# Performance work log

Hardware: AMD Instinct MI355X
Metric: run time of the kernel (lower is better)

## Reference

```python
import jax, jax.numpy as jnp
import numpy as np


def conv3x3(y, w, b):
    # y: [1, Cin, H, W], w: [Cout, Cin, 3, 3] -> [1, Cout, H, W], stride 1, pad 1
    out = jax.lax.conv_general_dilated(
        y, w, window_strides=(1, 1), padding='SAME',
        dimension_numbers=('NCHW', 'OIHW', 'NCHW'))
    return out + b[None, :, None, None]


def setup_inputs() -> dict:
    key = jax.random.key(0)
    ks = jax.random.split(key, 8)
    N, Cin, Cy, H, W, inter = 1024, 1024, 256, 128, 128, 256
    x = jax.random.normal(ks[0], (N, Cin), dtype=jnp.float32)
    y = jax.random.normal(ks[1], (1, Cy, H, W), dtype=jnp.float32)
    # weights initialized ~N(0, 0.01) as in the torch module; biases zero
    g_w = jax.random.normal(ks[2], (inter, Cy, 3, 3), dtype=jnp.float32) * 0.01
    g_b = jnp.zeros((inter,), dtype=jnp.float32)
    phi_w = jax.random.normal(ks[3], (inter, Cy, 3, 3), dtype=jnp.float32) * 0.01
    phi_b = jnp.zeros((inter,), dtype=jnp.float32)
    theta_w = jax.random.normal(ks[4], (inter, Cin), dtype=jnp.float32) * 0.01
    theta_b = jnp.zeros((inter,), dtype=jnp.float32)
    concat_w = jax.random.normal(ks[5], (1, 2 * inter, 1, 1), dtype=jnp.float32) * 0.01
    gamma = jnp.ones((1,), dtype=jnp.float32)  # torch inits 0; use 1 for nontrivial output
    return {"x": x, "y": y, "g_w": g_w, "g_b": g_b, "phi_w": phi_w,
            "phi_b": phi_b, "theta_w": theta_w, "theta_b": theta_b,
            "concat_w": concat_w, "gamma": gamma}


def reference(x, y, g_w, g_b, phi_w, phi_b, theta_w, theta_b, concat_w, gamma):
    inter = g_w.shape[0]
    H, W = y.shape[2], y.shape[3]
    g_y = conv3x3(y, g_w, g_b)          # [1, inter, H, W]
    phi_y = conv3x3(y, phi_w, phi_b)    # [1, inter, H, W]
    theta_x = x @ theta_w.T + theta_b   # [N, inter]
    # 1x1 conv over cat([theta repeated, phi repeated], dim=1) decomposes exactly
    # (linearity of the 1x1 conv, no bias) into two dot products + broadcast add,
    # avoiding the [N, 2*inter, H, W] materialization.
    w = concat_w[0, :, 0, 0]            # [2*inter]
    w_t, w_p = w[:inter], w[inter:]
    s_theta = theta_x @ w_t             # [N]
    s_phi = jnp.einsum('chw,c->hw', phi_y[0], w_p).reshape(-1)  # [H*W]
    f = jax.nn.softmax(s_theta[:, None] + s_phi[None, :], axis=1)  # [N, H*W]
    # g_y.squeeze() -> [inter,H,W]; permute(1,2,0).view(H*W, inter)
    g_flat = jnp.transpose(g_y[0], (1, 2, 0)).reshape(H * W, inter)
    z = gamma * (f @ g_flat)            # [N, inter]
    return z
```

## Files before the change

### kernel.cpp

```cpp
#include <hip/hip_runtime.h>

#define HWDIM 128
#define NPIX  (HWDIM * HWDIM)
#define CY    256
#define INTER 256
#define KTAPS 9
#define WEN   (CY * KTAPS)
#define NPART 64
#define NW1   8
#define NRG   4


__device__ __forceinline__ float wave_red_sum(float v) {
    #pragma unroll
    for (int s = 32; s > 0; s >>= 1) v += __shfl_down(v, s, 64);
    return v;
}
__device__ __forceinline__ float wave_red_max(float v) {
    #pragma unroll
    for (int s = 32; s > 0; s >>= 1) v = fmaxf(v, __shfl_down(v, s, 64));
    return v;
}

__global__ void k1_wepart(const float* __restrict__ phi_w,
                          const float* __restrict__ concat_w,
                          float* __restrict__ we_part) {
    int b = blockIdx.x, t = threadIdx.x;
    int og = b >> 3, cg = b & 7;
    int o = og * 256 + t;
    const float* pw = phi_w + o;
    float acc = 0.f;
    #pragma unroll 8
    for (int c = cg * 32; c < cg * 32 + 32; ++c)
        acc = fmaf(concat_w[INTER + c], pw[c * WEN], acc);
    we_part[cg * WEN + o] = acc;
}

template <int CPG>
__global__ void k2a_taps(const float* __restrict__ y,
                         const float* __restrict__ we_part,
                         float* __restrict__ A_part) {
    __shared__ float swe[CPG * KTAPS];
    int t = threadIdx.x;
    int pg = blockIdx.x & 63;
    int cg = blockIdx.x >> 6;

    for (int i = t; i < CPG * KTAPS; i += 256) {
        float s = 0.f;
        #pragma unroll
        for (int p = 0; p < NW1; ++p)
            s += we_part[p * WEN + cg * CPG * KTAPS + i];
        swe[i] = s;
    }
    __syncthreads();

    int pix = pg * 256 + t;
    float acc[KTAPS];
    #pragma unroll
    for (int k = 0; k < KTAPS; ++k) acc[k] = 0.f;

    const float* yp = y + (size_t)cg * CPG * NPIX + pix;
    #pragma unroll 4
    for (int ch = 0; ch < CPG; ++ch) {
        float yv = yp[ch * NPIX];
        const float* wk = swe + ch * KTAPS;
        #pragma unroll
        for (int k = 0; k < KTAPS; ++k)
            acc[k] = fmaf(wk[k], yv, acc[k]);
    }
    #pragma unroll
    for (int k = 0; k < KTAPS; ++k)
        A_part[(size_t)(cg * KTAPS + k) * NPIX + pix] = acc[k];
}

template <int NCS>
__global__ void k2b_sphi(const float* __restrict__ A_part,
                         float* __restrict__ sphi,
                         float* __restrict__ partials) {
    __shared__ float s4[4];
    __shared__ float sM;
    int t = threadIdx.x, wid = t >> 6, lane = t & 63;
    int pix = blockIdx.x * 256 + t;
    int h = pix >> 7, w = pix & 127;

    float acc = 0.f;
    #pragma unroll
    for (int kh = 0; kh < 3; ++kh) {
        int hh = h + kh - 1;
        if ((unsigned)hh >= (unsigned)HWDIM) continue;
        #pragma unroll
        for (int kw = 0; kw < 3; ++kw) {
            int ww = w + kw - 1;
            if ((unsigned)ww >= (unsigned)HWDIM) continue;
            int idx = hh * HWDIM + ww;
            int k = kh * 3 + kw;
            #pragma unroll
            for (int cg = 0; cg < NCS; ++cg)
                acc += A_part[(size_t)(cg * KTAPS + k) * NPIX + idx];
        }
    }
    sphi[pix] = acc;

    float m = wave_red_max(acc);
    if (lane == 0) s4[wid] = m;
    __syncthreads();
    if (t == 0) sM = fmaxf(fmaxf(s4[0], s4[1]), fmaxf(s4[2], s4[3]));
    __syncthreads();
    float M = sM;
    float e = expf(acc - M);
    float s = wave_red_sum(e);
    if (lane == 0) s4[wid] = s;
    __syncthreads();
    if (t == 0) {
        partials[2 * blockIdx.x]     = M;
        partials[2 * blockIdx.x + 1] = s4[0] + s4[1] + s4[2] + s4[3];
    }
}

__global__ void k3b_merge(const float* __restrict__ partials,
                          float* __restrict__ MS) {
    int t = threadIdx.x;
    float m = partials[2 * t], s = partials[2 * t + 1];
    float mr = wave_red_max(m);
    float M = __shfl(mr, 0, 64);
    float sv = s * expf(m - M);
    float S = wave_red_sum(sv);
    if (t == 0) { MS[0] = M; MS[1] = 1.f / S; }
}

__global__ void k4_q(const float* __restrict__ y,
                     const float* __restrict__ sphi,
                     const float* __restrict__ MS,
                     float* __restrict__ q_part) {
    __shared__ float sp[34 * 130];
    __shared__ float sq4[4][KTAPS];
    int cy = blockIdx.x & 255;
    int rg = blockIdx.x >> 8;
    int t = threadIdx.x;

    float M = MS[0], invS = MS[1];

    for (int i = t; i < 34 * 130; i += 256) {
        int r = i / 130, col = i - r * 130;
        int gr = rg * 32 + r - 1, gc = col - 1;
        float v = 0.f;
        if ((unsigned)gr < HWDIM && (unsigned)gc < HWDIM)
            v = expf(sphi[gr * HWDIM + gc] - M) * invS;
        sp[i] = v;
    }
    __syncthreads();

    const float* yc = y + (size_t)cy * NPIX;
    float acc[KTAPS];
    #pragma unroll
    for (int k = 0; k < KTAPS; ++k) acc[k] = 0.f;
    int c = t & 127, vg = t >> 7;

    for (int j = 0; j < 4; ++j) {
        int lr0 = vg * 4 + j * 8;
        float pv[6][3];
        #pragma unroll
        for (int u = 0; u < 6; ++u)
            #pragma unroll
            for (int v = 0; v < 3; ++v)
                pv[u][v] = sp[(lr0 + u) * 130 + c + v];
        #pragma unroll
        for (int dr = 0; dr < 4; ++dr) {
            float yv = yc[(rg * 32 + lr0 + dr) * HWDIM + c];
            #pragma unroll
            for (int kh = 0; kh < 3; ++kh)
                #pragma unroll
                for (int kw = 0; kw < 3; ++kw)
                    acc[kh * 3 + kw] = fmaf(pv[dr + 2 - kh][2 - kw], yv,
                                            acc[kh * 3 + kw]);
        }
    }

    int wid = t >> 6, lane = t & 63;
    #pragma unroll
    for (int k = 0; k < KTAPS; ++k) {
        float v = wave_red_sum(acc[k]);
        if (lane == 0) sq4[wid][k] = v;
    }
    __syncthreads();
    if (t < KTAPS)
        q_part[rg * WEN + cy * KTAPS + t] =
            sq4[0][t] + sq4[1][t] + sq4[2][t] + sq4[3][t];
}

__global__ void k5_row(const float* __restrict__ g_w,
                       const float* __restrict__ g_b,
                       const float* __restrict__ gamma,
                       const float* __restrict__ q_part,
                       float* __restrict__ row) {
    __shared__ float sq[WEN];
    __shared__ float s4[4];
    int t = threadIdx.x, c = blockIdx.x;
    for (int i = t; i < WEN; i += 256) {
        float s = 0.f;
        #pragma unroll
        for (int rg = 0; rg < NRG; ++rg) s += q_part[rg * WEN + i];
        sq[i] = s;
    }
    __syncthreads();

    const float* gw = g_w + (size_t)c * WEN;
    float acc = 0.f;
    for (int o = t; o < WEN; o += 256) acc = fmaf(gw[o], sq[o], acc);
    float v = wave_red_sum(acc);
    int wid = t >> 6, lane = t & 63;
    if (lane == 0) s4[wid] = v;
    __syncthreads();
    if (t == 0) row[c] = gamma[0] * (g_b[c] + s4[0] + s4[1] + s4[2] + s4[3]);
}

__global__ void k6_bcast(const float* __restrict__ row, float* __restrict__ out,
                         int out_size) {
    __shared__ float sr[256];
    sr[threadIdx.x] = row[threadIdx.x];
    __syncthreads();
    int gid = blockIdx.x * 256 + threadIdx.x;
    if (gid < out_size) out[gid] = sr[threadIdx.x];
}

extern "C" void kernel_launch(void* const* d_in, const int* in_sizes, int n_in,
                              void* d_out, int out_size, void* d_ws, size_t ws_size,
                              hipStream_t stream) {
    const float* y        = (const float*)d_in[1];
    const float* g_w      = (const float*)d_in[2];
    const float* g_b      = (const float*)d_in[3];
    const float* phi_w    = (const float*)d_in[4];
    const float* concat_w = (const float*)d_in[8];
    const float* gamma    = (const float*)d_in[9];
    float* out = (float*)d_out;

    const bool big = ws_size >= (size_t)(6u << 20);
    const int  ncs = big ? 8 : 2;

    float* ws       = (float*)d_ws;
    float* we_part  = ws;
    float* A_part   = we_part + NW1 * WEN;
    float* sphi     = A_part + (size_t)ncs * KTAPS * NPIX;
    float* partials = sphi + NPIX;
    float* MS       = partials + 2 * NPART;
    float* q_part   = MS + 16;
    float* row      = q_part + NRG * WEN;
    (void)in_sizes; (void)n_in;

    hipLaunchKernelGGL(k1_wepart, dim3(72), dim3(256), 0, stream,
                       phi_w, concat_w, we_part);
    if (big)
        hipLaunchKernelGGL(k2a_taps<32>,  dim3(64 * 8), dim3(256), 0, stream,
                           y, we_part, A_part);
    else
        hipLaunchKernelGGL(k2a_taps<128>, dim3(64 * 2), dim3(256), 0, stream,
                           y, we_part, A_part);
    if (big)
        hipLaunchKernelGGL(k2b_sphi<8>, dim3(NPART), dim3(256), 0, stream,
                           A_part, sphi, partials);
    else
        hipLaunchKernelGGL(k2b_sphi<2>, dim3(NPART), dim3(256), 0, stream,
                           A_part, sphi, partials);
    hipLaunchKernelGGL(k3b_merge, dim3(1), dim3(64), 0, stream, partials, MS);
    hipLaunchKernelGGL(k4_q, dim3(NRG * CY), dim3(256), 0, stream,
                       y, sphi, MS, q_part);
    hipLaunchKernelGGL(k5_row, dim3(CY), dim3(256), 0, stream,
                       g_w, g_b, gamma, q_part, row);
    hipLaunchKernelGGL(k6_bcast, dim3((out_size + 255) / 256), dim3(256), 0,
                       stream, row, out, out_size);
}
```

Baseline: 121.1 us.

## Widen grids, fold softmax merge into q kernel, split row reduction

Raises parallelism across the small kernels. The phi-weight partial sums now use 288 blocks instead of 72, the s_phi stage uses 256 blocks with four waves splitting the channel groups, and the row reduction uses 512 blocks with two halves that the broadcast kernel combines. The separate single-block softmax-merge kernel is removed; each k4 block now redoes the merge of the 256 (max, sum) partials itself, which removes one launch but repeats that small reduction in every block. The small-workspace fallback path is dropped, so the code now always assumes the large workspace.

```diff
diff --git a/kernel.cpp b/kernel.cpp
--- a/kernel.cpp
+++ b/kernel.cpp
@@ -6,8 +6,10 @@
 #define INTER 256
 #define KTAPS 9
 #define WEN   (CY * KTAPS)
-#define NPART 64
-#define NW1   8
+#define NW1   32
+#define NCS   8
+#define CPG   32
+#define NPART2 256
 #define NRG   4
 
 
@@ -26,20 +28,21 @@
                           const float* __restrict__ concat_w,
                           float* __restrict__ we_part) {
     int b = blockIdx.x, t = threadIdx.x;
-    int og = b >> 3, cg = b & 7;
+    int cg = b / 9, og = b - cg * 9;
     int o = og * 256 + t;
     const float* pw = phi_w + o;
     float acc = 0.f;
-    #pragma unroll 8
-    for (int c = cg * 32; c < cg * 32 + 32; ++c)
+    #pragma unroll
+    for (int j = 0; j < 8; ++j) {
+        int c = cg * 8 + j;
         acc = fmaf(concat_w[INTER + c], pw[c * WEN], acc);
+    }
     we_part[cg * WEN + o] = acc;
 }
 
-template <int CPG>
 __global__ void k2a_taps(const float* __restrict__ y,
                          const float* __restrict__ we_part,
-                         float* __restrict__ A_part) {
+                         float* __restrict__ A) {
     __shared__ float swe[CPG * KTAPS];
     int t = threadIdx.x;
     int pg = blockIdx.x & 63;
@@ -70,75 +73,76 @@
     }
     #pragma unroll
     for (int k = 0; k < KTAPS; ++k)
-        A_part[(size_t)(cg * KTAPS + k) * NPIX + pix] = acc[k];
-}
-
-template <int NCS>
-__global__ void k2b_sphi(const float* __restrict__ A_part,
+        A[(size_t)(cg * KTAPS + k) * NPIX + pix] = acc[k];
+}
+
+__global__ void k2b_sphi(const float* __restrict__ A,
                          float* __restrict__ sphi,
                          float* __restrict__ partials) {
-    __shared__ float s4[4];
-    __shared__ float sM;
-    int t = threadIdx.x, wid = t >> 6, lane = t & 63;
-    int pix = blockIdx.x * 256 + t;
+    __shared__ float sred[256];
+    int t = threadIdx.x;
+    int tg = t >> 6, pl = t & 63;
+    int pix = blockIdx.x * 64 + pl;
     int h = pix >> 7, w = pix & 127;
 
+    int idx[KTAPS]; bool val[KTAPS];
+    #pragma unroll
+    for (int kh = 0; kh < 3; ++kh)
+        #pragma unroll
+        for (int kw = 0; kw < 3; ++kw) {
+            int hh = h + kh - 1, ww = w + kw - 1;
+            int k = kh * 3 + kw;
+            val[k] = ((unsigned)hh < HWDIM) & ((unsigned)ww < HWDIM);
+            idx[k] = hh * HWDIM + ww;
+        }
+
     float acc = 0.f;
     #pragma unroll
-    for (int kh = 0; kh < 3; ++kh) {
-        int hh = h + kh - 1;
-        if ((unsigned)hh >= (unsigned)HWDIM) continue;
-        #pragma unroll
-        for (int kw = 0; kw < 3; ++kw) {
-            int ww = w + kw - 1;
-            if ((unsigned)ww >= (unsigned)HWDIM) continue;
-            int idx = hh * HWDIM + ww;
-            int k = kh * 3 + kw;
-            #pragma unroll
-            for (int cg = 0; cg < NCS; ++cg)
-                acc += A_part[(size_t)(cg * KTAPS + k) * NPIX + idx];
-        }
-    }
-    sphi[pix] = acc;
-
-    float m = wave_red_max(acc);
-    if (lane == 0) s4[wid] = m;
-    __syncthreads();
-    if (t == 0) sM = fmaxf(fmaxf(s4[0], s4[1]), fmaxf(s4[2], s4[3]));
-    __syncthreads();
-    float M = sM;
-    float e = expf(acc - M);
-    float s = wave_red_sum(e);
-    if (lane == 0) s4[wid] = s;
-    __syncthreads();
-    if (t == 0) {
-        partials[2 * blockIdx.x]     = M;
-        partials[2 * blockIdx.x + 1] = s4[0] + s4[1] + s4[2] + s4[3];
-    }
-}
-
-__global__ void k3b_merge(const float* __restrict__ partials,
-                          float* __restrict__ MS) {
-    int t = threadIdx.x;
-    float m = partials[2 * t], s = partials[2 * t + 1];
-    float mr = wave_red_max(m);
-    float M = __shfl(mr, 0, 64);
-    float sv = s * expf(m - M);
-    float S = wave_red_sum(sv);
-    if (t == 0) { MS[0] = M; MS[1] = 1.f / S; }
+    for (int cc = 0; cc < 2; ++cc) {
+        const float* Ab = A + (size_t)(tg * 2 + cc) * KTAPS * NPIX;
+        #pragma unroll
+        for (int k = 0; k < KTAPS; ++k)
+            if (val[k]) acc += Ab[(size_t)k * NPIX + idx[k]];
+    }
+    sred[t] = acc;
+    __syncthreads();
+
+    if (t < 64) {
+        float v = sred[t] + sred[t + 64] + sred[t + 128] + sred[t + 192];
+        sphi[blockIdx.x * 64 + t] = v;
+        float m = wave_red_max(v);
+        float M = __shfl(m, 0, 64);
+        float e = expf(v - M);
+        float s = wave_red_sum(e);
+        if (t == 0) {
+            partials[2 * blockIdx.x]     = M;
+            partials[2 * blockIdx.x + 1] = s;
+        }
+    }
 }
 
 __global__ void k4_q(const float* __restrict__ y,
                      const float* __restrict__ sphi,
-                     const float* __restrict__ MS,
+                     const float* __restrict__ partials,
                      float* __restrict__ q_part) {
     __shared__ float sp[34 * 130];
+    __shared__ float s4m[4], s4s[4];
     __shared__ float sq4[4][KTAPS];
     int cy = blockIdx.x & 255;
     int rg = blockIdx.x >> 8;
     int t = threadIdx.x;
-
-    float M = MS[0], invS = MS[1];
+    int wid = t >> 6, lane = t & 63;
+
+    float m = partials[2 * t], s = partials[2 * t + 1];
+    float wm = wave_red_max(m);
+    if (lane == 0) s4m[wid] = wm;
+    __syncthreads();
+    float M = fmaxf(fmaxf(s4m[0], s4m[1]), fmaxf(s4m[2], s4m[3]));
+    float sv = s * expf(m - M);
+    float wsum = wave_red_sum(sv);
+    if (lane == 0) s4s[wid] = wsum;
+    __syncthreads();
+    float invS = 1.f / (s4s[0] + s4s[1] + s4s[2] + s4s[3]);
 
     for (int i = t; i < 34 * 130; i += 256) {
         int r = i / 130, col = i - r * 130;
@@ -176,7 +180,6 @@
         }
     }
 
-    int wid = t >> 6, lane = t & 63;
     #pragma unroll
     for (int k = 0; k < KTAPS; ++k) {
         float v = wave_red_sum(acc[k]);
@@ -189,38 +192,42 @@
 }
 
 __global__ void k5_row(const float* __restrict__ g_w,
-                       const float* __restrict__ g_b,
-                       const float* __restrict__ gamma,
                        const float* __restrict__ q_part,
-                       float* __restrict__ row) {
-    __shared__ float sq[WEN];
+                       float* __restrict__ row_part) {
     __shared__ float s4[4];
-    int t = threadIdx.x, c = blockIdx.x;
-    for (int i = t; i < WEN; i += 256) {
-        float s = 0.f;
-        #pragma unroll
-        for (int rg = 0; rg < NRG; ++rg) s += q_part[rg * WEN + i];
-        sq[i] = s;
-    }
-    __syncthreads();
+    int t = threadIdx.x;
+    int c = blockIdx.x & 255, half = blockIdx.x >> 8;
+    int base = half * (WEN / 2);
 
     const float* gw = g_w + (size_t)c * WEN;
     float acc = 0.f;
-    for (int o = t; o < WEN; o += 256) acc = fmaf(gw[o], sq[o], acc);
+    #pragma unroll
+    for (int j = 0; j < 5; ++j) {
+        int o = base + j * 256 + t;
+        if (o < base + WEN / 2) {
+            float qv = q_part[o] + q_part[WEN + o] +
+                       q_part[2 * WEN + o] + q_part[3 * WEN + o];
+            acc = fmaf(gw[o], qv, acc);
+        }
+    }
     float v = wave_red_sum(acc);
     int wid = t >> 6, lane = t & 63;
     if (lane == 0) s4[wid] = v;
     __syncthreads();
-    if (t == 0) row[c] = gamma[0] * (g_b[c] + s4[0] + s4[1] + s4[2] + s4[3]);
-}
-
-__global__ void k6_bcast(const float* __restrict__ row, float* __restrict__ out,
-                         int out_size) {
+    if (t == 0)
+        row_part[half * 256 + c] = s4[0] + s4[1] + s4[2] + s4[3];
+}
+
+__global__ void k6_bcast(const float* __restrict__ row_part,
+                         const float* __restrict__ g_b,
+                         const float* __restrict__ gamma,
+                         float* __restrict__ out, int out_size) {
     __shared__ float sr[256];
-    sr[threadIdx.x] = row[threadIdx.x];
-    __syncthreads();
-    int gid = blockIdx.x * 256 + threadIdx.x;
-    if (gid < out_size) out[gid] = sr[threadIdx.x];
+    int t = threadIdx.x;
+    sr[t] = gamma[0] * (g_b[t] + row_part[t] + row_part[256 + t]);
+    __syncthreads();
+    int gid = blockIdx.x * 256 + t;
+    if (gid < out_size) out[gid] = sr[t];
 }
 
 extern "C" void kernel_launch(void* const* d_in, const int* in_sizes, int n_in,
@@ -234,38 +241,25 @@
     const float* gamma    = (const float*)d_in[9];
     float* out = (float*)d_out;
 
-    const bool big = ws_size >= (size_t)(6u << 20);
-    const int  ncs = big ? 8 : 2;
-
     float* ws       = (float*)d_ws;
     float* we_part  = ws;
-    float* A_part   = we_part + NW1 * WEN;
-    float* sphi     = A_part + (size_t)ncs * KTAPS * NPIX;
+    float* A        = we_part + NW1 * WEN;
+    float* sphi     = A + (size_t)NCS * KTAPS * NPIX;
     float* partials = sphi + NPIX;
-    float* MS       = partials + 2 * NPART;
-    float* q_part   = MS + 16;
-    float* row      = q_part + NRG * WEN;
-    (void)in_sizes; (void)n_in;
-
-    hipLaunchKernelGGL(k1_wepart, dim3(72), dim3(256), 0, stream,
+    float* q_part   = partials + 2 * NPART2;
+    float* row_part = q_part + NRG * WEN;
+    (void)in_sizes; (void)n_in; (void)ws_size;
+
+    hipLaunchKernelGGL(k1_wepart, dim3(288),      dim3(256), 0, stream,
                        phi_w, concat_w, we_part);
-    if (big)
-        hipLaunchKernelGGL(k2a_taps<32>,  dim3(64 * 8), dim3(256), 0, stream,
-                           y, we_part, A_part);
-    else
-        hipLaunchKernelGGL(k2a_taps<128>, dim3(64 * 2), dim3(256), 0, stream,
-                           y, we_part, A_part);
-    if (big)
-        hipLaunchKernelGGL(k2b_sphi<8>, dim3(NPART), dim3(256), 0, stream,
-                           A_part, sphi, partials);
-    else
-        hipLaunchKernelGGL(k2b_sphi<2>, dim3(NPART), dim3(256), 0, stream,
-                           A_part, sphi, partials);
-    hipLaunchKernelGGL(k3b_merge, dim3(1), dim3(64), 0, stream, partials, MS);
-    hipLaunchKernelGGL(k4_q, dim3(NRG * CY), dim3(256), 0, stream,
-                       y, sphi, MS, q_part);
-    hipLaunchKernelGGL(k5_row, dim3(CY), dim3(256), 0, stream,
-                       g_w, g_b, gamma, q_part, row);
-    hipLaunchKernelGGL(k6_bcast, dim3((out_size + 255) / 256), dim3(256), 0,
-                       stream, row, out, out_size);
-}
+    hipLaunchKernelGGL(k2a_taps,  dim3(64 * NCS), dim3(256), 0, stream,
+                       y, we_part, A);
+    hipLaunchKernelGGL(k2b_sphi,  dim3(NPART2),   dim3(256), 0, stream,
+                       A, sphi, partials);
+    hipLaunchKernelGGL(k4_q,      dim3(NRG * CY), dim3(256), 0, stream,
+                       y, sphi, partials, q_part);
+    hipLaunchKernelGGL(k5_row,    dim3(512),      dim3(256), 0, stream,
+                       g_w, q_part, row_part);
+    hipLaunchKernelGGL(k6_bcast,  dim3((out_size + 255) / 256), dim3(256), 0,
+                       stream, row_part, g_b, gamma, out, out_size);
+}
```

After: 117.1 us. 3.3% less time.
